# Optimization experiments

Hardware: AMD Instinct MI355X
Metric: run time of the kernel (lower is better)

## Reference

```python
import jax, jax.numpy as jnp
import numpy as np

DELTA = 1e-6
B, INPUT, N, WL, R = 32, 1024, 1024, 64, 4
IFACE = WL * R + 3 * WL + 5 * R + 3  # 471


def setup_inputs() -> dict:
    key = jax.random.key(0)
    ks = jax.random.split(key, 9)
    return {
        "x": jax.random.normal(ks[0], (B, INPUT), jnp.float32),
        "W_if": jax.random.normal(ks[1], (INPUT, IFACE), jnp.float32) * 0.02,
        "b_if": jnp.zeros((IFACE,), jnp.float32),
        "memory": jax.random.normal(ks[2], (B, N, WL), jnp.float32) * 0.1,
        "link_matrix": jax.random.uniform(ks[3], (B, 1, N, N), jnp.float32) * 1e-3,
        "precedence": jax.random.uniform(ks[4], (B, 1, N), jnp.float32) * 1e-2,
        "read_weights": jax.random.uniform(ks[5], (B, R, N), jnp.float32) / N,
        "write_weights": jax.random.uniform(ks[6], (B, 1, N), jnp.float32) / N,
        "usage": jax.random.uniform(ks[7], (B, N), jnp.float32),
    }


def _content(memory, keys, strengths):
    # cosine-similarity content addressing; memory [b,N,W], keys [b,h,W]
    mn = memory / (jnp.linalg.norm(memory, axis=-1, keepdims=True) + DELTA)
    kn = keys / (jnp.linalg.norm(keys, axis=-1, keepdims=True) + DELTA)
    sim = jnp.einsum('bhw,bnw->bhn', kn, mn)
    return jax.nn.softmax(sim * strengths[..., None], axis=-1)


def reference(x, W_if, b_if, memory, link_matrix, precedence, read_weights, write_weights, usage):
    b = x.shape[0]
    xi = x @ W_if + b_if  # [b, IFACE]

    # --- parse interface vector (offsets per the torch module) ---
    o = 0
    read_keys = jnp.tanh(xi[:, o:o + R * WL].reshape(b, R, WL)); o += R * WL
    read_strengths = jax.nn.softplus(xi[:, o:o + R]); o += R            # [b,r]
    write_key = jnp.tanh(xi[:, o:o + WL].reshape(b, 1, WL)); o += WL
    write_strength = jax.nn.softplus(xi[:, o:o + 1]); o += 1            # [b,1]
    erase_vector = jax.nn.sigmoid(xi[:, o:o + WL].reshape(b, 1, WL)); o += WL
    write_vector = jnp.tanh(xi[:, o:o + WL].reshape(b, 1, WL)); o += WL
    free_gates = jax.nn.sigmoid(xi[:, o:o + R]); o += R                 # [b,r]
    allocation_gate = jax.nn.sigmoid(xi[:, o:o + 1]); o += 1            # [b,1]
    write_gate = jax.nn.sigmoid(xi[:, o:o + 1]); o += 1                 # [b,1]
    read_modes = jax.nn.softmax(xi[:, o:o + 3 * R].reshape(b, R, 3), axis=-1)

    # --- write phase ---
    wcw = _content(memory, write_key, write_strength)  # [b,1,N]

    # usage update
    u = usage + (1.0 - usage) * (1.0 - jnp.prod(1.0 - write_weights, axis=1))
    psi = jnp.prod(1.0 - free_gates[:, :, None] * read_weights, axis=1)
    u = u * psi

    # allocation via ascending sort + exclusive cumprod, then unsort
    u = DELTA + (1.0 - DELTA) * u
    perm = jnp.argsort(u, axis=1)                       # ascending usage order (phi)
    sorted_u = jnp.take_along_axis(u, perm, axis=1)
    ones_col = jnp.ones((b, 1), u.dtype)
    prod_su = jnp.cumprod(jnp.concatenate([ones_col, sorted_u], axis=1), axis=1)[:, :-1]
    sorted_alloc = (1.0 - sorted_u) * prod_su
    inv_perm = jnp.argsort(perm, axis=1)                # phi_rev: inverse permutation
    alloc = jnp.take_along_axis(sorted_alloc, inv_perm, axis=1)[:, None, :]  # [b,1,N]

    # write weighting
    ag = allocation_gate[..., None]
    wg = write_gate[..., None]
    ww = wg * (ag * alloc + (1.0 - ag) * wcw)           # [b,1,N]

    # memory erase + write (h = 1 write head)
    new_memory = memory * (1.0 - jnp.einsum('bhn,bhw->bnw', ww, erase_vector)) \
                 + jnp.einsum('bhn,bhw->bnw', ww, write_vector)

    # link matrix update (NxN outer-product, zero diagonal)
    ww_i = ww[:, :, :, None]                            # [b,1,N,1]
    ww_j = ww[:, :, None, :]                            # [b,1,1,N]
    prec_j = precedence[:, :, None, :]                  # [b,1,1,N]
    new_link = (1.0 - ww_i - ww_j) * link_matrix + ww_i * prec_j
    eye_mask = 1.0 - jnp.eye(N, dtype=new_link.dtype)
    new_link = new_link * eye_mask[None, None, :, :]

    # precedence update
    new_prec = (1.0 - jnp.sum(ww, axis=-1, keepdims=True)) * precedence + ww

    # --- read phase ---
    fwd_w = jnp.einsum('bhij,brj->bri', new_link, read_weights)   # forward links
    bwd_w = jnp.einsum('bhji,brj->bri', new_link, read_weights)   # backward links
    crw = _content(new_memory, read_keys, read_strengths)         # [b,r,N]
    new_rw = read_modes[..., 0:1] * bwd_w + read_modes[..., 1:2] * crw + read_modes[..., 2:3] * fwd_w
    read_vectors = jnp.einsum('brn,bnw->brw', new_rw, new_memory)  # [b,r,W]
    return read_vectors
```

## Files before the change

### kernel.cpp

```cpp
#include <hip/hip_runtime.h>
#include <math.h>

#define DELTA_ 1e-6f
#define IFACE_ 471
#define XI_STRIDE 480

#define OFF_XI    0
#define OFF_RKN   15360
#define OFF_RS    23552
#define OFF_ER    23680
#define OFF_WV    25728
#define OFF_RM    27776
#define OFF_WW    28160
#define OFF_WWRW  60928
#define OFF_PRD   192000
#define OFF_WRD   192128
#define OFF_INVN  192256
#define OFF_DIAG  225024
#define OFF_NM    257792
#define OFF_RAP   2354944
#define OFF_RBP   2617088
#define OFF_SAP   2879232
#define OFF_SBP   4976384

__device__ __forceinline__ float sigm_(float x){ return 1.f/(1.f+expf(-x)); }
__device__ __forceinline__ float softp_(float x){ return fmaxf(x,0.f)+log1pf(expf(-fabsf(x))); }
__device__ __forceinline__ float dot4_(float4 a, float4 b){ return a.x*b.x+a.y*b.y+a.z*b.z+a.w*b.w; }

__global__ __launch_bounds__(256) void k_xi(const float* __restrict__ x,
    const float* __restrict__ W, const float* __restrict__ bias,
    float* __restrict__ xi) {
  int b = blockIdx.x;
  int j0 = blockIdx.y*64;
  int t = threadIdx.x;
  int jl = t & 63, kq = t >> 6;
  __shared__ __align__(16) float sx[1024];
  __shared__ float s_part[256];
  for (int q=t; q<256; q+=256) ((float4*)sx)[q] = ((const float4*)(x + b*1024))[q];
  __syncthreads();
  int j = j0 + jl;
  int jc = j < IFACE_ ? j : IFACE_-1;
  float acc = 0.f;
  const float* Wp = W + (size_t)kq*256*IFACE_ + jc;
  #pragma unroll 4
  for (int k=0;k<256;++k) acc += sx[kq*256+k]*Wp[(size_t)k*IFACE_];
  s_part[t] = acc;
  __syncthreads();
  if (t < 64 && (j0+t) < IFACE_) {
    xi[b*XI_STRIDE + j0+t] = s_part[t]+s_part[64+t]+s_part[128+t]+s_part[192+t] + bias[j0+t];
  }
}

__global__ __launch_bounds__(256) void k_batch(
    const float* __restrict__ xi, const float* __restrict__ memory,
    const float* __restrict__ usage, const float* __restrict__ read_w,
    const float* __restrict__ write_w, const float* __restrict__ precedence,
    float* __restrict__ rkn, float* __restrict__ rs, float* __restrict__ er,
    float* __restrict__ wv, float* __restrict__ rm, float* __restrict__ ww_out,
    float* __restrict__ wwrw, float* __restrict__ prd, float* __restrict__ wrd) {
  int b = blockIdx.x; int t = threadIdx.x;
  int lane = t & 63; int wave = t >> 6;
  __shared__ float s_act[472];
  __shared__ __align__(16) float s_key[64];
  __shared__ float s_wcw[1024];
  __shared__ unsigned long long s_k64[1024];
  __shared__ float s_ps[1024];
  __shared__ float s_alloc[1024];
  __shared__ float s_red[32];
  __shared__ float s_bc[2];

  for (int q = t; q < IFACE_; q += 256) {
    float v = xi[b*XI_STRIDE+q];
    float a;
    if      (q < 256) a = tanhf(v);
    else if (q < 260) a = softp_(v);
    else if (q < 324) a = tanhf(v);
    else if (q < 325) a = softp_(v);
    else if (q < 389) a = sigm_(v);
    else if (q < 453) a = tanhf(v);
    else if (q < 459) a = sigm_(v);
    else              a = v;
    s_act[q] = a;
  }
  __syncthreads();
  if (t < 4) {
    float m0=s_act[459+3*t], m1=s_act[460+3*t], m2=s_act[461+3*t];
    float mx=fmaxf(m0,fmaxf(m1,m2));
    float e0=expf(m0-mx), e1=expf(m1-mx), e2=expf(m2-mx);
    float s=e0+e1+e2;
    rm[b*12+3*t+0]=e0/s; rm[b*12+3*t+1]=e1/s; rm[b*12+3*t+2]=e2/s;
  }
  if (t < 64) { er[b*64+t]=s_act[325+t]; wv[b*64+t]=s_act[389+t]; }
  {
    int r = wave;
    float v = s_act[r*64+lane];
    float ss = v*v;
    for (int off=32; off; off>>=1) ss += __shfl_xor(ss, off);
    rkn[((size_t)b*4+r)*64+lane] = v / (sqrtf(ss)+DELTA_);
    if (lane==0) rs[b*4+r] = s_act[256+r];
  }
  if (wave==0) {
    float v = s_act[260+lane];
    float ss=v*v;
    for (int off=32; off; off>>=1) ss += __shfl_xor(ss, off);
    s_key[lane] = v/(sqrtf(ss)+DELTA_);
  }
  __syncthreads();
  float wstr = s_act[324], agv = s_act[457], wgv = s_act[458];

  for (int n=t; n<1024; n+=256) {
    const float4* row = (const float4*)(memory + ((size_t)b*1024+n)*64);
    float dot=0.f, nn2=0.f;
    #pragma unroll
    for (int w4=0; w4<16; ++w4) {
      float4 m4 = row[w4];
      float4 k4 = ((const float4*)s_key)[w4];
      dot += dot4_(m4,k4);
      nn2 += dot4_(m4,m4);
    }
    s_wcw[n] = dot/(sqrtf(nn2)+DELTA_) * wstr;
  }
  __syncthreads();
  {
    float lm=-1e30f;
    for (int n=t;n<1024;n+=256) lm=fmaxf(lm,s_wcw[n]);
    for (int off=32;off;off>>=1) lm=fmaxf(lm,__shfl_xor(lm,off));
    if (lane==0) s_red[wave]=lm;
    __syncthreads();
    if (t==0) s_bc[0]=fmaxf(fmaxf(s_red[0],s_red[1]),fmaxf(s_red[2],s_red[3]));
    __syncthreads();
    float mx=s_bc[0], ls=0.f;
    for (int n=t;n<1024;n+=256){ float e=expf(s_wcw[n]-mx); s_wcw[n]=e; ls+=e; }
    for (int off=32;off;off>>=1) ls+=__shfl_xor(ls,off);
    if (lane==0) s_red[wave]=ls;
    __syncthreads();
    if (t==0) s_bc[1]=s_red[0]+s_red[1]+s_red[2]+s_red[3];
    __syncthreads();
    float inv=1.f/s_bc[1];
    for (int n=t;n<1024;n+=256) s_wcw[n]*=inv;
  }
  __syncthreads();

  for (int n=t; n<1024; n+=256) {
    float us = usage[b*1024+n];
    float wwi = write_w[b*1024+n];
    float u = us + (1.f-us)*wwi;
    float psi = 1.f;
    #pragma unroll
    for (int r=0;r<4;++r) psi *= (1.f - s_act[453+r]*read_w[((size_t)b*4+r)*1024+n]);
    u *= psi;
    u = DELTA_ + (1.f-DELTA_)*u;
    unsigned int ub = __float_as_uint(u);
    s_k64[n] = ((unsigned long long)ub<<32) | (unsigned int)n;
  }

  for (int k=2; k<=1024; k<<=1) {
    for (int j=k>>1; j>0; j>>=1) {
      __syncthreads();
      for (int idx=t; idx<1024; idx+=256) {
        int partner = idx ^ j;
        if (partner > idx) {
          unsigned long long a=s_k64[idx], c=s_k64[partner];
          bool asc = ((idx & k) == 0);
          bool sw = asc ? (a > c) : (a < c);
          if (sw) { s_k64[idx]=c; s_k64[partner]=a; }
        }
      }
    }
  }
  __syncthreads();

  for (int n=t;n<1024;n+=256) s_ps[n] = __uint_as_float((unsigned int)(s_k64[n]>>32));
  __syncthreads();
  for (int off=1; off<1024; off<<=1) {
    float tmp[4];
    #pragma unroll
    for (int m=0;m<4;++m){ int n=t+256*m; tmp[m] = (n>=off)? s_ps[n-off] : 1.f; }
    __syncthreads();
    #pragma unroll
    for (int m=0;m<4;++m){ int n=t+256*m; s_ps[n] *= tmp[m]; }
    __syncthreads();
  }
  for (int n=t;n<1024;n+=256) {
    unsigned long long kv = s_k64[n];
    float su = __uint_as_float((unsigned int)(kv>>32));
    int oi = (int)(kv & 0xffffffffu);
    float prod = (n==0)?1.f:s_ps[n-1];
    s_alloc[oi] = (1.f-su)*prod;
  }
  __syncthreads();

  float pp[4]={0,0,0,0}, wp[4]={0,0,0,0};
  for (int n=t;n<1024;n+=256) {
    float w_ = wgv*(agv*s_alloc[n] + (1.f-agv)*s_wcw[n]);
    ww_out[b*1024+n]=w_;
    float pn = precedence[b*1024+n];
    #pragma unroll
    for (int r=0;r<4;++r){
      float rwv = read_w[((size_t)b*4+r)*1024+n];
      wwrw[((size_t)b*4+r)*1024+n] = w_*rwv;
      pp[r] += pn*rwv;
      wp[r] += w_*rwv;
    }
  }
  #pragma unroll
  for (int r=0;r<4;++r){
    for (int off=32;off;off>>=1){ pp[r]+=__shfl_xor(pp[r],off); wp[r]+=__shfl_xor(wp[r],off); }
  }
  if (lane==0){
    #pragma unroll
    for (int r=0;r<4;++r){ s_red[wave*8+r]=pp[r]; s_red[wave*8+4+r]=wp[r]; }
  }
  __syncthreads();
  if (t<4)              prd[b*4+t]   = s_red[t]+s_red[8+t]+s_red[16+t]+s_red[24+t];
  else if (t<8){ int r=t-4; wrd[b*4+r] = s_red[4+r]+s_red[12+r]+s_red[20+r]+s_red[28+r]; }
}

__global__ __launch_bounds__(256) void k_newmem(const float* __restrict__ memory,
    const float* __restrict__ ww, const float* __restrict__ er,
    const float* __restrict__ wv, float* __restrict__ newmem, float* __restrict__ invn) {
  int b = blockIdx.x;
  int n0 = blockIdx.y*64;
  int t = threadIdx.x;
  int lane16 = t & 15, rl = t >> 4;
  __shared__ float s_ww[64];
  __shared__ __align__(16) float s_er[64];
  __shared__ __align__(16) float s_wv[64];
  if (t < 64) s_ww[t] = ww[b*1024 + n0 + t];
  else if (t < 128) s_er[t-64] = er[b*64 + (t-64)];
  else if (t < 192) s_wv[t-128] = wv[b*64 + (t-128)];
  __syncthreads();
  float4 e4 = ((const float4*)s_er)[lane16];
  float4 v4 = ((const float4*)s_wv)[lane16];
  #pragma unroll
  for (int p=0;p<4;++p) {
    int rloc = p*16 + rl;
    int row = n0 + rloc;
    float wn = s_ww[rloc];
    size_t i4 = ((size_t)b*1024+row)*16 + lane16;
    float4 m4 = ((const float4*)memory)[i4];
    float4 nv;
    nv.x = m4.x*(1.f-wn*e4.x) + wn*v4.x;
    nv.y = m4.y*(1.f-wn*e4.y) + wn*v4.y;
    nv.z = m4.z*(1.f-wn*e4.z) + wn*v4.z;
    nv.w = m4.w*(1.f-wn*e4.w) + wn*v4.w;
    ((float4*)newmem)[i4] = nv;
    float ss = dot4_(nv,nv);
    ss += __shfl_xor(ss,1); ss += __shfl_xor(ss,2);
    ss += __shfl_xor(ss,4); ss += __shfl_xor(ss,8);
    if (lane16==0) invn[b*1024+row] = 1.f/(sqrtf(ss)+DELTA_);
  }
}

__global__ __launch_bounds__(256) void k_scan(const float* __restrict__ L,
    const float* __restrict__ read_w, const float* __restrict__ wwrw,
    float* __restrict__ RAp, float* __restrict__ RBp,
    float* __restrict__ SAp, float* __restrict__ SBp,
    float* __restrict__ diag) {
  int b = blockIdx.x, rc = blockIdx.y, cc = blockIdx.z;
  int i0 = rc*64;
  int q = threadIdx.x;
  int r = q>>6, lc = q&63;
  __shared__ __align__(16) float RM[64*68];
  __shared__ __align__(16) float CM[64*68];
  __shared__ __align__(16) float s_wc[256], s_uc[256];
  __shared__ __align__(16) float s_wr[256], s_ur[256];
  s_wr[q] = read_w[((size_t)b*4+r)*1024 + i0 + lc];
  s_ur[q] = wwrw  [((size_t)b*4+r)*1024 + i0 + lc];
  const float4* L4 = (const float4*)(L + (size_t)b*1048576);
  float4 pre[4]; float wpA, wpB;
  {
    int tc0 = cc*512;
    #pragma unroll
    for (int m=0;m<4;++m){
      int flat = q + 256*m;
      int row = flat>>4, c4 = flat&15;
      pre[m] = L4[(size_t)(i0+row)*256 + (tc0>>2) + c4];
    }
    wpA = read_w[((size_t)b*4+r)*1024 + tc0 + lc];
    wpB = wwrw  [((size_t)b*4+r)*1024 + tc0 + lc];
  }
  float pa=0.f, pb=0.f;
  for (int t=0;t<8;++t) {
    int tc0 = cc*512 + t*64;
    __syncthreads();
    #pragma unroll
    for (int m=0;m<4;++m){
      int flat = q + 256*m;
      int row = flat>>4, c4 = flat&15;
      ((float4*)RM)[row*17 + c4] = pre[m];
      const float* p = (const float*)&pre[m];
      #pragma unroll
      for (int j=0;j<4;++j) CM[(4*c4+j)*68 + row] = p[j];
    }
    s_wc[q] = wpA; s_uc[q] = wpB;
    __syncthreads();
    if (t<7){
      int nc0 = tc0 + 64;
      #pragma unroll
      for (int m=0;m<4;++m){
        int flat = q + 256*m;
        int row = flat>>4, c4 = flat&15;
        pre[m] = L4[(size_t)(i0+row)*256 + (nc0>>2) + c4];
      }
      wpA = read_w[((size_t)b*4+r)*1024 + nc0 + lc];
      wpB = wwrw  [((size_t)b*4+r)*1024 + nc0 + lc];
    }
    if (i0 == tc0 && q < 64) diag[b*1024 + i0 + q] = RM[q*68 + q];
    {
      const float4* RM4 = (const float4*)RM;
      const float4* w4p = (const float4*)(s_wc + r*64);
      const float4* u4p = (const float4*)(s_uc + r*64);
      #pragma unroll
      for (int c4=0;c4<16;++c4){
        float4 a4 = RM4[lc*17 + c4];
        pa += dot4_(a4, w4p[c4]);
        pb += dot4_(a4, u4p[c4]);
      }
    }
    {
      const float4* CM4 = (const float4*)CM;
      const float4* w4p = (const float4*)(s_wr + r*64);
      const float4* u4p = (const float4*)(s_ur + r*64);
      float sa=0.f, sb=0.f;
      #pragma unroll
      for (int i4=0;i4<16;++i4){
        float4 c4v = CM4[lc*17 + i4];
        sa += dot4_(c4v, w4p[i4]);
        sb += dot4_(c4v, u4p[i4]);
      }
      SAp[(((size_t)(b*16+rc))*4+r)*1024 + tc0 + lc] = sa;
      SBp[(((size_t)(b*16+rc))*4+r)*1024 + tc0 + lc] = sb;
    }
  }
  RAp[(((size_t)(b*2+cc))*4+r)*1024 + i0 + lc] = pa;
  RBp[(((size_t)(b*2+cc))*4+r)*1024 + i0 + lc] = pb;
}

__global__ __launch_bounds__(256) void k_read(
    const float* __restrict__ newmem, const float* __restrict__ invn,
    const float* __restrict__ rkn, const float* __restrict__ rs,
    const float* __restrict__ rm, const float* __restrict__ RAp,
    const float* __restrict__ RBp, const float* __restrict__ SAp,
    const float* __restrict__ SBp, const float* __restrict__ ww,
    const float* __restrict__ precedence, const float* __restrict__ read_w,
    const float* __restrict__ diag, const float* __restrict__ prd,
    const float* __restrict__ wrd, float* __restrict__ out) {
  int b=blockIdx.x, r=blockIdx.y;
  int t=threadIdx.x, lane=t&63, wave=t>>6;
  int lane16 = t & 15, rl = t >> 4;
  __shared__ __align__(16) float s_key[64];
  __shared__ float s_arr[1024];
  __shared__ float s_red[4];
  __shared__ float s_bc[2];
  __shared__ __align__(16) float4 s_acc[16][16];
  if (t<64) s_key[t]=rkn[((size_t)b*4+r)*64+t];
  __syncthreads();
  float rstr = rs[b*4+r];
  float4 key4 = ((const float4*)s_key)[lane16];
  for (int p=0;p<64;++p) {
    int row = p*16 + rl;
    float4 m4 = ((const float4*)newmem)[((size_t)b*1024+row)*16 + lane16];
    float d = dot4_(m4, key4);
    d += __shfl_xor(d,1); d += __shfl_xor(d,2);
    d += __shfl_xor(d,4); d += __shfl_xor(d,8);
    if (lane16==0) s_arr[row] = d * invn[b*1024+row] * rstr;
  }
  __syncthreads();
  {
    float lm=-1e30f;
    for (int n=t;n<1024;n+=256) lm=fmaxf(lm,s_arr[n]);
    for (int off=32;off;off>>=1) lm=fmaxf(lm,__shfl_xor(lm,off));
    if (lane==0) s_red[wave]=lm;
    __syncthreads();
    if (t==0) s_bc[0]=fmaxf(fmaxf(s_red[0],s_red[1]),fmaxf(s_red[2],s_red[3]));
    __syncthreads();
    float mx=s_bc[0], ls=0.f;
    for (int n=t;n<1024;n+=256){ float e=expf(s_arr[n]-mx); s_arr[n]=e; ls+=e; }
    for (int off=32;off;off>>=1) ls+=__shfl_xor(ls,off);
    if (lane==0) s_red[wave]=ls;
    __syncthreads();
    if (t==0) s_bc[1]=s_red[0]+s_red[1]+s_red[2]+s_red[3];
    __syncthreads();
    float inv=1.f/s_bc[1];
    for (int n=t;n<1024;n+=256) s_arr[n]*=inv;
  }
  __syncthreads();
  float m0=rm[b*12+r*3+0], m1=rm[b*12+r*3+1], m2=rm[b*12+r*3+2];
  float pd=prd[b*4+r], wd=wrd[b*4+r];
  for (int n=t;n<1024;n+=256) {
    float ra=0.f, rb=0.f;
    #pragma unroll
    for (int cc=0;cc<2;++cc){
      ra += RAp[(((size_t)(b*2+cc))*4+r)*1024+n];
      rb += RBp[(((size_t)(b*2+cc))*4+r)*1024+n];
    }
    float sa=0.f, sb=0.f;
    #pragma unroll
    for (int rc=0;rc<16;++rc){
      sa+=SAp[(((size_t)(b*16+rc))*4+r)*1024+n];
      sb+=SBp[(((size_t)(b*16+rc))*4+r)*1024+n];
    }
    float w_ = ww[b*1024+n];
    float pn = precedence[b*1024+n];
    float rwv= read_w[((size_t)b*4+r)*1024+n];
    float dg = diag[b*1024+n];
    float fwd = (1.f-w_)*ra - rb + w_*pd - ((1.f-2.f*w_)*dg + w_*pn)*rwv;
    float bwd = (1.f-w_)*sa - sb + pn*(wd - w_*rwv) - (1.f-2.f*w_)*dg*rwv;
    float crw = s_arr[n];
    __syncthreads();
    s_arr[n] = m0*bwd + m1*crw + m2*fwd;
    __syncthreads();
  }
  __syncthreads();
  float4 acc = {0,0,0,0};
  for (int p=0;p<64;++p) {
    int row = p*16 + rl;
    float4 m4 = ((const float4*)newmem)[((size_t)b*1024+row)*16 + lane16];
    float s = s_arr[row];
    acc.x += s*m4.x; acc.y += s*m4.y; acc.z += s*m4.z; acc.w += s*m4.w;
  }
  s_acc[rl][lane16] = acc;
  __syncthreads();
  if (t < 16) {
    float4 tot = {0,0,0,0};
    #pragma unroll
    for (int g=0; g<16; ++g) {
      float4 v = s_acc[g][t];
      tot.x+=v.x; tot.y+=v.y; tot.z+=v.z; tot.w+=v.w;
    }
    ((float4*)(out + (b*4+r)*64))[t] = tot;
  }
}

extern "C" void kernel_launch(void* const* d_in, const int* in_sizes, int n_in,
                              void* d_out, int out_size, void* d_ws, size_t ws_size,
                              hipStream_t stream) {
  const float* x      = (const float*)d_in[0];
  const float* W_if   = (const float*)d_in[1];
  const float* b_if   = (const float*)d_in[2];
  const float* memory = (const float*)d_in[3];
  const float* link   = (const float*)d_in[4];
  const float* prec   = (const float*)d_in[5];
  const float* read_w = (const float*)d_in[6];
  const float* write_w= (const float*)d_in[7];
  const float* usage  = (const float*)d_in[8];
  float* out = (float*)d_out;
  float* ws = (float*)d_ws;

  float* xi   = ws + OFF_XI;
  float* rkn  = ws + OFF_RKN;
  float* rs   = ws + OFF_RS;
  float* er   = ws + OFF_ER;
  float* wv   = ws + OFF_WV;
  float* rm   = ws + OFF_RM;
  float* wwp  = ws + OFF_WW;
  float* wwrw = ws + OFF_WWRW;
  float* prd  = ws + OFF_PRD;
  float* wrd  = ws + OFF_WRD;
  float* invn = ws + OFF_INVN;
  float* diag = ws + OFF_DIAG;
  float* nm   = ws + OFF_NM;
  float* RAp  = ws + OFF_RAP;
  float* RBp  = ws + OFF_RBP;
  float* SAp  = ws + OFF_SAP;
  float* SBp  = ws + OFF_SBP;

  k_xi<<<dim3(32,8), 256, 0, stream>>>(x, W_if, b_if, xi);
  k_batch<<<dim3(32), 256, 0, stream>>>(xi, memory, usage, read_w, write_w, prec,
                                        rkn, rs, er, wv, rm, wwp, wwrw, prd, wrd);
  k_scan<<<dim3(32,16,2), 256, 0, stream>>>(link, read_w, wwrw, RAp, RBp, SAp, SBp, diag);
  k_newmem<<<dim3(32,16), 256, 0, stream>>>(memory, wwp, er, wv, nm, invn);
  k_read<<<dim3(32,4), 256, 0, stream>>>(nm, invn, rkn, rs, rm, RAp, RBp, SAp, SBp,
                                         wwp, prec, read_w, diag, prd, wrd, out);
}
```

Before: 371.3 us.

## Rewrite link-matrix scan with column-per-thread loads and bf16 MFMA row products

The link-matrix scan kernel now has each thread stream one column of a 64x256 tile from global memory. Each thread accumulates the column-direction (backward) products in fp32 registers while writing a bf16 copy of the tile to shared memory. The row-direction (forward) products against the read and write weight vectors are then computed with 16x16x32 bf16 MFMA instructions instead of scalar float4 dot products over transposed shared-memory tiles. This removes the dual fp32 shared-memory transposes and the register prefetch pipeline, but drops precision to bf16 for the forward term and loses the explicit load/compute overlap.

```diff
diff --git a/kernel.cpp b/kernel.cpp
--- a/kernel.cpp
+++ b/kernel.cpp
@@ -23,9 +23,17 @@
 #define OFF_SAP   2879232
 #define OFF_SBP   4976384
 
+typedef __attribute__((ext_vector_type(8))) short short8;
+typedef __attribute__((ext_vector_type(4))) float f32x4;
+
 __device__ __forceinline__ float sigm_(float x){ return 1.f/(1.f+expf(-x)); }
 __device__ __forceinline__ float softp_(float x){ return fmaxf(x,0.f)+log1pf(expf(-fabsf(x))); }
 __device__ __forceinline__ float dot4_(float4 a, float4 b){ return a.x*b.x+a.y*b.y+a.z*b.z+a.w*b.w; }
+__device__ __forceinline__ unsigned short f2bf_(float x){
+  unsigned u = __float_as_uint(x);
+  unsigned r = (u + 0x7fffu + ((u>>16)&1u)) >> 16;
+  return (unsigned short)r;
+}
 
 __global__ __launch_bounds__(256) void k_xi(const float* __restrict__ x,
     const float* __restrict__ W, const float* __restrict__ bias,
@@ -259,82 +267,94 @@
     float* __restrict__ diag) {
   int b = blockIdx.x, rc = blockIdx.y, cc = blockIdx.z;
   int i0 = rc*64;
-  int q = threadIdx.x;
-  int r = q>>6, lc = q&63;
-  __shared__ __align__(16) float RM[64*68];
-  __shared__ __align__(16) float CM[64*68];
-  __shared__ __align__(16) float s_wc[256], s_uc[256];
-  __shared__ __align__(16) float s_wr[256], s_ur[256];
-  s_wr[q] = read_w[((size_t)b*4+r)*1024 + i0 + lc];
-  s_ur[q] = wwrw  [((size_t)b*4+r)*1024 + i0 + lc];
-  const float4* L4 = (const float4*)(L + (size_t)b*1048576);
-  float4 pre[4]; float wpA, wpB;
+  int c_base = cc*512;
+  int t = threadIdx.x;
+  int w = t>>6, l = t&63;
+
+  __shared__ unsigned short At[64*264];
+  __shared__ unsigned short BTs[16*264];
+  __shared__ __align__(16) float s_w8[64][8];
+
+  if (t < 64) {
+    #pragma unroll
+    for (int r=0;r<4;++r) {
+      s_w8[t][r]   = read_w[((size_t)b*4+r)*1024 + i0 + t];
+      s_w8[t][4+r] = wwrw  [((size_t)b*4+r)*1024 + i0 + t];
+    }
+  }
+  __syncthreads();
+
+  f32x4 acc = {0.f,0.f,0.f,0.f};
+
+  for (int tq=0; tq<2; ++tq) {
+    if (tq) __syncthreads();
+    int tile0 = c_base + tq*256;
+    const float* Lcol = L + (size_t)b*1048576 + (size_t)i0*1024 + tile0 + t;
+    float ca0=0,ca1=0,ca2=0,ca3=0, cb0=0,cb1=0,cb2=0,cb3=0;
+    int dl = i0 - tile0;
+    #pragma unroll 8
+    for (int i=0;i<64;++i) {
+      float v = Lcol[(size_t)i*1024];
+      float4 wA = *((const float4*)&s_w8[i][0]);
+      float4 wB = *((const float4*)&s_w8[i][4]);
+      ca0 += v*wA.x; ca1 += v*wA.y; ca2 += v*wA.z; ca3 += v*wA.w;
+      cb0 += v*wB.x; cb1 += v*wB.y; cb2 += v*wB.z; cb3 += v*wB.w;
+      At[i*264 + t] = f2bf_(v);
+      if (t - dl == i) diag[b*1024 + i0 + i] = v;
+    }
+    {
+      int gcol = tile0 + t;
+      SAp[(((size_t)(b*16+rc))*4+0)*1024 + gcol] = ca0;
+      SAp[(((size_t)(b*16+rc))*4+1)*1024 + gcol] = ca1;
+      SAp[(((size_t)(b*16+rc))*4+2)*1024 + gcol] = ca2;
+      SAp[(((size_t)(b*16+rc))*4+3)*1024 + gcol] = ca3;
+      SBp[(((size_t)(b*16+rc))*4+0)*1024 + gcol] = cb0;
+      SBp[(((size_t)(b*16+rc))*4+1)*1024 + gcol] = cb1;
+      SBp[(((size_t)(b*16+rc))*4+2)*1024 + gcol] = cb2;
+      SBp[(((size_t)(b*16+rc))*4+3)*1024 + gcol] = cb3;
+    }
+    {
+      int n = t & 15, kc = t >> 4;
+      unsigned int packed[8];
+      if (n < 8) {
+        const float* wp = (n < 4 ? read_w + ((size_t)b*4+n)*1024
+                                 : wwrw   + ((size_t)b*4+(n-4))*1024) + tile0 + kc*16;
+        #pragma unroll
+        for (int j=0;j<8;++j) {
+          unsigned short lo = f2bf_(wp[2*j]);
+          unsigned short hi = f2bf_(wp[2*j+1]);
+          packed[j] = (unsigned int)lo | ((unsigned int)hi << 16);
+        }
+      } else {
+        #pragma unroll
+        for (int j=0;j<8;++j) packed[j] = 0u;
+      }
+      unsigned int* dst = (unsigned int*)&BTs[n*264 + kc*16];
+      #pragma unroll
+      for (int j=0;j<8;++j) dst[j] = packed[j];
+    }
+    __syncthreads();
+    {
+      int m = l & 15, q = l >> 4;
+      #pragma unroll
+      for (int kb=0; kb<8; ++kb) {
+        short8 afrag = *((const short8*)&At[(16*w + m)*264 + kb*32 + q*8]);
+        short8 bfrag = *((const short8*)&BTs[m*264 + kb*32 + q*8]);
+        acc = __builtin_amdgcn_mfma_f32_16x16x32_bf16(afrag, bfrag, acc, 0, 0, 0);
+      }
+    }
+  }
   {
-    int tc0 = cc*512;
-    #pragma unroll
-    for (int m=0;m<4;++m){
-      int flat = q + 256*m;
-      int row = flat>>4, c4 = flat&15;
-      pre[m] = L4[(size_t)(i0+row)*256 + (tc0>>2) + c4];
-    }
-    wpA = read_w[((size_t)b*4+r)*1024 + tc0 + lc];
-    wpB = wwrw  [((size_t)b*4+r)*1024 + tc0 + lc];
-  }
-  float pa=0.f, pb=0.f;
-  for (int t=0;t<8;++t) {
-    int tc0 = cc*512 + t*64;
-    __syncthreads();
-    #pragma unroll
-    for (int m=0;m<4;++m){
-      int flat = q + 256*m;
-      int row = flat>>4, c4 = flat&15;
-      ((float4*)RM)[row*17 + c4] = pre[m];
-      const float* p = (const float*)&pre[m];
+    int n = l & 15, q = l >> 4;
+    if (n < 8) {
+      float* dst = (n < 4) ? (RAp + (((size_t)(b*2+cc))*4+n)*1024)
+                           : (RBp + (((size_t)(b*2+cc))*4+(n-4))*1024);
       #pragma unroll
-      for (int j=0;j<4;++j) CM[(4*c4+j)*68 + row] = p[j];
-    }
-    s_wc[q] = wpA; s_uc[q] = wpB;
-    __syncthreads();
-    if (t<7){
-      int nc0 = tc0 + 64;
-      #pragma unroll
-      for (int m=0;m<4;++m){
-        int flat = q + 256*m;
-        int row = flat>>4, c4 = flat&15;
-        pre[m] = L4[(size_t)(i0+row)*256 + (nc0>>2) + c4];
+      for (int reg=0; reg<4; ++reg) {
+        dst[i0 + 16*w + q*4 + reg] = acc[reg];
       }
-      wpA = read_w[((size_t)b*4+r)*1024 + nc0 + lc];
-      wpB = wwrw  [((size_t)b*4+r)*1024 + nc0 + lc];
-    }
-    if (i0 == tc0 && q < 64) diag[b*1024 + i0 + q] = RM[q*68 + q];
-    {
-      const float4* RM4 = (const float4*)RM;
-      const float4* w4p = (const float4*)(s_wc + r*64);
-      const float4* u4p = (const float4*)(s_uc + r*64);
-      #pragma unroll
-      for (int c4=0;c4<16;++c4){
-        float4 a4 = RM4[lc*17 + c4];
-        pa += dot4_(a4, w4p[c4]);
-        pb += dot4_(a4, u4p[c4]);
-      }
-    }
-    {
-      const float4* CM4 = (const float4*)CM;
-      const float4* w4p = (const float4*)(s_wr + r*64);
-      const float4* u4p = (const float4*)(s_ur + r*64);
-      float sa=0.f, sb=0.f;
-      #pragma unroll
-      for (int i4=0;i4<16;++i4){
-        float4 c4v = CM4[lc*17 + i4];
-        sa += dot4_(c4v, w4p[i4]);
-        sb += dot4_(c4v, u4p[i4]);
-      }
-      SAp[(((size_t)(b*16+rc))*4+r)*1024 + tc0 + lc] = sa;
-      SBp[(((size_t)(b*16+rc))*4+r)*1024 + tc0 + lc] = sb;
-    }
-  }
-  RAp[(((size_t)(b*2+cc))*4+r)*1024 + i0 + lc] = pa;
-  RBp[(((size_t)(b*2+cc))*4+r)*1024 + i0 + lc] = pb;
+    }
+  }
 }
 
 __global__ __launch_bounds__(256) void k_read(
```

Result: slower. 454.7 us (+22.5%).
